# Optimization experiments

Measured on AMD Instinct MI355X. Metric: run time of the kernel, lower is better.

The kernel has to match this reference:

```python
import jax, jax.numpy as jnp
import numpy as np

B, C, F_, T = 128, 8, 58, 249
RES_C = 24  # out_c * len('fct')


def conv1d(x, w, b, stride):
    # x: (B, Cin, L), w: (Cout, Cin, K)
    y = jax.lax.conv_general_dilated(x, w, (stride,), 'VALID',
                                     dimension_numbers=('NCH', 'OIH', 'NCH'))
    return y + b[None, :, None]


def attend(Q, K, V):
    # torch: softmax(Q @ K^T / sqrt(d_q), dim=1) @ V   (softmax over ROWS, dim=1)
    d = Q.shape[-1]
    scores = jnp.einsum('bnd,bmd->bnm', Q, K) / jnp.sqrt(jnp.asarray(d, Q.dtype))
    alpha = jax.nn.softmax(scores, axis=1)
    return jnp.einsum('bnm,bml->bnl', alpha, V)


def dyrelub(x, w1, b1, w2, b2):
    # standard DyReLU-B, k=2: coefs from global-avg-pooled features
    b_, c_ = x.shape[0], x.shape[1]
    theta = x.mean(axis=(2, 3))                       # (B, C)
    h = jax.nn.relu(theta @ w1.T + b1)
    theta = 2.0 * jax.nn.sigmoid(h @ w2.T + b2) - 1.0  # (B, 4C)
    lambdas = jnp.array([1.0, 1.0, 0.5, 0.5], dtype=x.dtype)
    init_v = jnp.array([1.0, 0.0, 0.0, 0.0], dtype=x.dtype)
    coefs = theta.reshape(b_, c_, 4) * lambdas + init_v  # (B,C,4)
    a = coefs[:, :, None, None, :2]
    bb = coefs[:, :, None, None, 2:]
    return jnp.max(x[..., None] * a + bb, axis=-1)


def setup_inputs():
    key = jax.random.key(0)
    ks = iter(jax.random.split(key, 48))

    def rn(shape, s=0.1):
        return jax.random.normal(next(ks), shape, dtype=jnp.float32) * s

    return {
        'x': jax.random.normal(next(ks), (B, C, F_, T), dtype=jnp.float32),
        'inp': jax.random.normal(next(ks), (B, 1, F_ + 2, T + 2), dtype=jnp.float32),
        'w_diff': rn((C, C)), 'b_diff': rn((C,)),
        'w_res': rn((RES_C, 1, 3, 3)), 'b_res': rn((RES_C,)),
        'bn_gamma': jnp.ones((RES_C,), jnp.float32), 'bn_beta': jnp.zeros((RES_C,), jnp.float32),
        'bn_mean': rn((RES_C,)),
        'bn_var': jax.random.uniform(next(ks), (RES_C,), jnp.float32, 0.5, 1.5),
        'dy_w1': rn((6, RES_C)), 'dy_b1': rn((6,)),
        'dy_w2': rn((4 * RES_C, 6)), 'dy_b2': rn((4 * RES_C,)),
        'wq': rn((C, C)), 'bq': rn((C,)),
        'wk': rn((C, C)), 'bk': rn((C,)),
        'fq0_w': rn((F_, F_, 1)), 'fq0_b': rn((F_,)),
        'fk0_w': rn((F_, F_, 1)), 'fk0_b': rn((F_,)),
        'cq0_w': rn((C, C, 1)), 'cq0_b': rn((C,)),
        'ck0_w': rn((C, C, 1)), 'ck0_b': rn((C,)),
        'tq0_w': rn((T, T, 1)), 'tq0_b': rn((T,)),
        'tk0_w': rn((T, T, 1)), 'tk0_b': rn((T,)),
        'tq1_w': rn((T, T, 2)), 'tq1_b': rn((T,)),
        'tk1_w': rn((T, T, 2)), 'tk1_b': rn((T,)),
    }


def reference(x, inp, w_diff, b_diff, w_res, b_res, bn_gamma, bn_beta, bn_mean, bn_var,
              dy_w1, dy_b1, dy_w2, dy_b2, wq, bq, wk, bk,
              fq0_w, fq0_b, fk0_w, fk0_b, cq0_w, cq0_b, ck0_w, ck0_b,
              tq0_w, tq0_b, tk0_w, tk0_b, tq1_w, tq1_b, tk1_w, tk1_b):
    Bx = x.shape[0]
    # ---- differ branch (temporal difference via 1x1 conv) ----
    x_t_fea = x[..., :-1]                 # (B,C,F,T-1)
    first_t = x[..., :1]                  # (B,C,F,1)
    x_conv = jnp.einsum('oc,bcft->boft', w_diff, x) + b_diff[None, :, None, None]
    x_query = x_conv[..., 1:] - x_t_fea
    differ = jnp.concatenate([first_t, x_query], axis=-1)  # (B,C,F,T)

    # ---- residual branch: conv3x3 -> BN(eval) -> DyReLU-B ----
    xr = jax.lax.conv_general_dilated(inp, w_res, (1, 1), 'VALID',
                                      dimension_numbers=('NCHW', 'OIHW', 'NCHW'))
    xr = xr + b_res[None, :, None, None]
    inv = jax.lax.rsqrt(bn_var + 1e-5)
    xr = (xr - bn_mean[None, :, None, None]) * (inv * bn_gamma)[None, :, None, None] \
         + bn_beta[None, :, None, None]
    xr = dyrelub(xr, dy_w1, dy_b1, dy_w2, dy_b2)   # (B,24,F,T)

    # ---- multi-view multi-scale attention ----
    Q = jnp.einsum('oc,bcft->boft', wq, differ) + bq[None, :, None, None]
    K = jnp.einsum('oc,bcft->boft', wk, differ) + bk[None, :, None, None]
    V = differ

    # f view: raw reshape (B,C,F,T) -> (B,F,C*T)
    Qf = Q.reshape(Bx, F_, C * T); Kf = K.reshape(Bx, F_, C * T); Vf = V.reshape(Bx, F_, C * T)
    a_f = attend(Qf, Kf, Vf)
    a_f = a_f + attend(conv1d(Qf, fq0_w, fq0_b, 1), conv1d(Kf, fk0_w, fk0_b, 1), Vf)
    a_f = a_f.reshape(Bx, C, F_, T)

    # c view: (B,C,F*T)
    Qc = Q.reshape(Bx, C, F_ * T); Kc = K.reshape(Bx, C, F_ * T); Vc = V.reshape(Bx, C, F_ * T)
    a_c = attend(Qc, Kc, Vc)
    a_c = a_c + attend(conv1d(Qc, cq0_w, cq0_b, 1), conv1d(Kc, ck0_w, ck0_b, 1), Vc)
    a_c = a_c.reshape(Bx, C, F_, T)

    # t view: (B,T,C*F)
    Qt = Q.reshape(Bx, T, C * F_); Kt = K.reshape(Bx, T, C * F_); Vt = V.reshape(Bx, T, C * F_)
    a_t = attend(Qt, Kt, Vt)
    a_t = a_t + attend(conv1d(Qt, tq0_w, tq0_b, 1), conv1d(Kt, tk0_w, tk0_b, 1), Vt)
    a_t = a_t + attend(conv1d(Qt, tq1_w, tq1_b, 2), conv1d(Kt, tk1_w, tk1_b, 2), Vt)
    a_t = a_t.reshape(Bx, C, F_, T)

    atten_differ = jnp.concatenate([a_f, a_c, a_t], axis=1)  # (B,24,F,T)
    return atten_differ + xr
```

## Files before the change

kernel.cpp:

```cpp
#include <hip/hip_runtime.h>
#include <cmath>

#define Bn   128
#define Cn   8
#define Fn   58
#define Tn   249
#define RCn  24
#define FT   14442
#define CFT  115536
#define OUTB 346608
#define IH   60
#define IW   251

__global__ void k_differ_qk(const float* __restrict__ x,
                            const float* __restrict__ w_diff, const float* __restrict__ b_diff,
                            const float* __restrict__ wq, const float* __restrict__ bq,
                            const float* __restrict__ wk, const float* __restrict__ bk,
                            float* __restrict__ V, float* __restrict__ Q, float* __restrict__ K) {
    int gid = blockIdx.x * blockDim.x + threadIdx.x;
    if (gid >= Bn * FT) return;
    int b  = gid / FT;
    int ft = gid % FT;
    int t  = ft % Tn;
    const float* xb = x + (size_t)b * CFT + ft;

    float xv[Cn], d[Cn];
    #pragma unroll
    for (int c = 0; c < Cn; c++) xv[c] = xb[c * FT];

    if (t == 0) {
        #pragma unroll
        for (int c = 0; c < Cn; c++) d[c] = xv[c];
    } else {
        #pragma unroll
        for (int o = 0; o < Cn; o++) {
            float s = b_diff[o];
            #pragma unroll
            for (int c = 0; c < Cn; c++) s += w_diff[o * Cn + c] * xv[c];
            d[o] = s - xb[o * FT - 1];
        }
    }

    float* Vb = V + (size_t)b * CFT + ft;
    float* Qb = Q + (size_t)b * CFT + ft;
    float* Kb = K + (size_t)b * CFT + ft;
    #pragma unroll
    for (int o = 0; o < Cn; o++) {
        Vb[o * FT] = d[o];
        float q = bq[o], k = bk[o];
        #pragma unroll
        for (int c = 0; c < Cn; c++) { q += wq[o * Cn + c] * d[c]; k += wk[o * Cn + c] * d[c]; }
        Qb[o * FT] = q;
        Kb[o * FT] = k;
    }
}

template<int AN, int RG, int GW, int VL>
__global__ void __launch_bounds__(256, 4)
k_gemm(const float* __restrict__ A, long long aStride, int aLd,
       const float* __restrict__ bias,
       const float* __restrict__ V, long long vStride, int dv,
       float* __restrict__ out, long long oStride, int add,
       int gx, int gy)
{
    constexpr int TPG = 256 / GW;
    constexpr int RGA = (RG + 3) & ~3;
    constexpr int RGP = GW * RGA + 4;
    __shared__ float As[64][RGP];

    int nblk = gridDim.x;
    int bid  = blockIdx.x;
    if ((nblk & 7) == 0) {
        int cpx = nblk >> 3;
        bid = (bid & 7) * cpx + (bid >> 3);
    }
    int gxy = gx * gy;
    int b   = bid / gxy;
    int rem = bid - b * gxy;
    int jb  = (rem / gx) * (GW * RG);
    int g   = threadIdx.x / TPG;
    int cl  = threadIdx.x % TPG;
    int j0  = jb + g * RG;
    int l   = (rem % gx) * (TPG * VL) + cl * VL;
    bool act = (l + VL <= dv);

    const float* Ab = A + (size_t)b * aStride;
    const float* Vb = V + (size_t)b * vStride + l;

    float acc[RG][VL];
    #pragma unroll
    for (int j = 0; j < RG; j++)
        #pragma unroll
        for (int e = 0; e < VL; e++) acc[j][e] = 0.f;

    for (int m0 = 0; m0 < AN; m0 += 64) {
        int mc = min(64, AN - m0);
        for (int idx = threadIdx.x; idx < GW * RG * 64; idx += 256) {
            int j = idx >> 6, mi = idx & 63;
            float w = 0.f;
            if (jb + j < AN && mi < mc) w = Ab[(size_t)(jb + j) * aLd + m0 + mi];
            As[mi][(j / RG) * RGA + (j % RG)] = w;
        }
        __syncthreads();
        if (act) {
            const float* Vp = Vb + (size_t)m0 * dv;
            auto LD = [&](int i) -> float4 {
                const float* p = Vp + (size_t)min(i, mc - 1) * dv;
                if constexpr (VL == 4) {
                    return *(const float4*)p;
                } else {
                    float2 t = *(const float2*)p;
                    return make_float4(t.x, t.y, 0.f, 0.f);
                }
            };
            auto FMA = [&](int mm, float4 x) {
                const float* w = &As[mm][g * RGA];
                #pragma unroll
                for (int j = 0; j < RG; j++) {
                    float wv = w[j];
                    acc[j][0] += wv * x.x;
                    if constexpr (VL >= 2) acc[j][1] += wv * x.y;
                    if constexpr (VL >= 4) {
                        acc[j][2] += wv * x.z;
                        acc[j][3] += wv * x.w;
                    }
                }
            };
            float4 p0 = LD(0), p1 = LD(1), p2 = LD(2), p3 = LD(3);
            int mm = 0;
            for (; mm + 4 <= mc; mm += 4) {
                FMA(mm + 0, p0); p0 = LD(mm + 4);
                FMA(mm + 1, p1); p1 = LD(mm + 5);
                FMA(mm + 2, p2); p2 = LD(mm + 6);
                FMA(mm + 3, p3); p3 = LD(mm + 7);
            }
            if (mm     < mc) FMA(mm,     p0);
            if (mm + 1 < mc) FMA(mm + 1, p1);
            if (mm + 2 < mc) FMA(mm + 2, p2);
        }
        __syncthreads();
    }

    if (!act) return;
    float* ob = out + (size_t)b * oStride + l;
    #pragma unroll
    for (int j = 0; j < RG; j++) {
        if (j0 + j < AN) {
            float bv = bias ? bias[j0 + j] : 0.f;
            float* op = ob + (size_t)(j0 + j) * dv;
            if (add) {
                #pragma unroll
                for (int e = 0; e < VL; e++) op[e] += acc[j][e] + bv;
            } else {
                if constexpr (VL == 4) {
                    *(float4*)op = make_float4(acc[j][0] + bv, acc[j][1] + bv,
                                               acc[j][2] + bv, acc[j][3] + bv);
                } else {
                    *(float2*)op = make_float2(acc[j][0] + bv, acc[j][1] + bv);
                }
            }
        }
    }
}

template<int AN, int RGW>
__global__ void __launch_bounds__(256, 4)
k_gemm_s2d(const float* __restrict__ Wa, const float* __restrict__ ba,
           const float* __restrict__ Xa, float* __restrict__ Oa,
           const float* __restrict__ Wb, const float* __restrict__ bb_,
           const float* __restrict__ Xb_, float* __restrict__ Ob,
           long long xStride, int d_in, int d_out, long long oStride, int gy)
{
    constexpr int BR = 4 * RGW;
    __shared__ float Ws[64][2 * BR + 4];

    int nblk = gridDim.x;
    int bid  = blockIdx.x;
    if ((nblk & 7) == 0) {
        int cpx = nblk >> 3;
        bid = (bid & 7) * cpx + (bid >> 3);
    }
    int half = (bid >= Bn * gy);
    if (half) bid -= Bn * gy;
    const float* W    = half ? Wb  : Wa;
    const float* bias = half ? bb_ : ba;
    const float* X    = half ? Xb_ : Xa;
    float*       Og   = half ? Ob  : Oa;

    int b    = bid / gy;
    int jb   = (bid % gy) * BR;
    int w    = threadIdx.x >> 6;
    int lane = threadIdx.x & 63;
    int j0   = jb + w * RGW;
    int l4   = lane * 4;
    bool act = l4 < d_out;

    const float* Xb = X + (size_t)b * xStride + 2 * l4;

    float acc[RGW][4];
    #pragma unroll
    for (int j = 0; j < RGW; j++)
        #pragma unroll
        for (int e = 0; e < 4; e++) acc[j][e] = 0.f;

    for (int m0 = 0; m0 < AN; m0 += 64) {
        int mc = min(64, AN - m0);
        for (int idx = threadIdx.x; idx < 2 * BR * 64; idx += 256) {
            int mi = idx & 63, rest = idx >> 6;
            int rj = rest >> 1, tap = rest & 1;
            float wv = 0.f;
            if (jb + rj < AN && mi < mc)
                wv = W[((size_t)(jb + rj) * AN + m0 + mi) * 2 + tap];
            Ws[mi][2 * rj + tap] = wv;
        }
        __syncthreads();
        if (act) {
            const float* Xp = Xb + (size_t)m0 * d_in;
            auto FMAS = [&](int mm, float4 x0, float4 x1) {
                const float* wrow = &Ws[mm][2 * (w * RGW)];
                #pragma unroll
                for (int j = 0; j < RGW; j++) {
                    float w0 = wrow[2 * j], w1 = wrow[2 * j + 1];
                    acc[j][0] += w0 * x0.x + w1 * x0.y;
                    acc[j][1] += w0 * x0.z + w1 * x0.w;
                    acc[j][2] += w0 * x1.x + w1 * x1.y;
                    acc[j][3] += w0 * x1.z + w1 * x1.w;
                }
            };
            if (mc == 64) {
                auto LDU = [&](int i, float4& a, float4& bb) {
                    const float* p = Xp + (size_t)i * d_in;
                    a = *(const float4*)p; bb = *(const float4*)(p + 4);
                };
                float4 a0, b0, a1, b1, a2, b2, a3, b3;
                LDU(0, a0, b0); LDU(1, a1, b1); LDU(2, a2, b2); LDU(3, a3, b3);
                int mm = 0;
                for (; mm < 60; mm += 4) {
                    FMAS(mm + 0, a0, b0); LDU(mm + 4, a0, b0);
                    FMAS(mm + 1, a1, b1); LDU(mm + 5, a1, b1);
                    FMAS(mm + 2, a2, b2); LDU(mm + 6, a2, b2);
                    FMAS(mm + 3, a3, b3); LDU(mm + 7, a3, b3);
                }
                FMAS(60, a0, b0); FMAS(61, a1, b1);
                FMAS(62, a2, b2); FMAS(63, a3, b3);
            } else {
                auto LDP = [&](int i, float4& a, float4& bb) {
                    const float* p = Xp + (size_t)min(i, mc - 1) * d_in;
                    a = *(const float4*)p; bb = *(const float4*)(p + 4);
                };
                float4 a0, b0, a1, b1, a2, b2, a3, b3;
                LDP(0, a0, b0); LDP(1, a1, b1); LDP(2, a2, b2); LDP(3, a3, b3);
                int mm = 0;
                for (; mm + 4 <= mc; mm += 4) {
                    FMAS(mm + 0, a0, b0); LDP(mm + 4, a0, b0);
                    FMAS(mm + 1, a1, b1); LDP(mm + 5, a1, b1);
                    FMAS(mm + 2, a2, b2); LDP(mm + 6, a2, b2);
                    FMAS(mm + 3, a3, b3); LDP(mm + 7, a3, b3);
                }
                if (mm     < mc) FMAS(mm,     a0, b0);
                if (mm + 1 < mc) FMAS(mm + 1, a1, b1);
                if (mm + 2 < mc) FMAS(mm + 2, a2, b2);
            }
        }
        __syncthreads();
    }

    if (!act) return;
    float* ob = Og + (size_t)b * oStride + l4;
    #pragma unroll
    for (int j = 0; j < RGW; j++) {
        if (j0 + j < AN) {
            float bv = bias[j0 + j];
            *(float4*)(ob + (size_t)(j0 + j) * d_out) =
                make_float4(acc[j][0] + bv, acc[j][1] + bv,
                            acc[j][2] + bv, acc[j][3] + bv);
        }
    }
}

__global__ void __launch_bounds__(256, 4)
k_scores128(const float* __restrict__ Q, const float* __restrict__ K,
            float* __restrict__ S, int n, int d, int sQ) {
    __shared__ float Qs[16][132];
    __shared__ float Ks[16][132];
    int b  = blockIdx.z;
    int r0 = blockIdx.x * 128, c0 = blockIdx.y * 128;
    int tid = threadIdx.x;
    int tx = tid & 15, ty = tid >> 4;
    int lrow = tid >> 1;
    int lk   = (tid & 1) * 8;
    const float* Qr = Q + (size_t)b * sQ + (size_t)min(r0 + lrow, n - 1) * d;
    const float* Kr = K + (size_t)b * sQ + (size_t)min(c0 + lrow, n - 1) * d;

    float acc[8][8] = {};
    for (int kk = 0; kk < d; kk += 16) {
        #pragma unroll
        for (int h = 0; h < 2; h++) {
            int g = kk + lk + h * 4;
            float4 qv = make_float4(0.f, 0.f, 0.f, 0.f);
            float4 kv = make_float4(0.f, 0.f, 0.f, 0.f);
            if (g + 4 <= d) {
                qv = *(const float4*)(Qr + g);
                kv = *(const float4*)(Kr + g);
            }
            int kb = lk + h * 4;
            Qs[kb + 0][lrow] = qv.x; Qs[kb + 1][lrow] = qv.y;
            Qs[kb + 2][lrow] = qv.z; Qs[kb + 3][lrow] = qv.w;
            Ks[kb + 0][lrow] = kv.x; Ks[kb + 1][lrow] = kv.y;
            Ks[kb + 2][lrow] = kv.z; Ks[kb + 3][lrow] = kv.w;
        }
        __syncthreads();
        #pragma unroll
        for (int k = 0; k < 16; k++) {
            float4 qa = *(const float4*)&Qs[k][ty * 8];
            float4 qb = *(const float4*)&Qs[k][ty * 8 + 4];
            float4 ka = *(const float4*)&Ks[k][tx * 8];
            float4 kb4 = *(const float4*)&Ks[k][tx * 8 + 4];
            float aq[8] = {qa.x, qa.y, qa.z, qa.w, qb.x, qb.y, qb.z, qb.w};
            float ak[8] = {ka.x, ka.y, ka.z, ka.w, kb4.x, kb4.y, kb4.z, kb4.w};
            #pragma unroll
            for (int i = 0; i < 8; i++)
                #pragma unroll
                for (int j = 0; j < 8; j++) acc[i][j] += aq[i] * ak[j];
        }
        __syncthreads();
    }
    float* Sb = S + (size_t)b * n * n;
    #pragma unroll
    for (int i = 0; i < 8; i++) {
        int r = r0 + ty * 8 + i;
        if (r < n) {
            #pragma unroll
            for (int j = 0; j < 8; j++) {
                int c = c0 + tx * 8 + j;
                if (c < n) Sb[(size_t)r * n + c] = acc[i][j];
            }
        }
    }
}

__global__ void __launch_bounds__(256)
k_scores_sk(const float* __restrict__ Q, const float* __restrict__ K,
            float* __restrict__ SP, int n, int d, int kz_n, int chunk, int sQ) {
    __shared__ float Qs[16][68];
    __shared__ float Ks[16][68];
    int bz = blockIdx.z;
    int b  = bz / kz_n, kz = bz % kz_n;
    int k0 = kz * chunk, k1 = min(d, k0 + chunk);
    int r0 = blockIdx.x * 64, c0 = blockIdx.y * 64;
    int tx = threadIdx.x & 15, ty = threadIdx.x >> 4;
    int lrow = threadIdx.x >> 2;
    int lk   = (threadIdx.x & 3) * 4;
    const float* Qr = Q + (size_t)b * sQ + (size_t)min(r0 + lrow, n - 1) * d;
    const float* Kr = K + (size_t)b * sQ + (size_t)min(c0 + lrow, n - 1) * d;
    bool qok = (r0 + lrow) < n;
    bool kok = (c0 + lrow) < n;
    float acc[4][4] = {};

    for (int kk = k0; kk < k1; kk += 16) {
        #pragma unroll
        for (int u = 0; u < 4; u++) {
            int gk = kk + lk + u;
            bool gv = gk < k1;
            Qs[lk + u][lrow] = (qok && gv) ? Qr[gk] : 0.f;
            Ks[lk + u][lrow] = (kok && gv) ? Kr[gk] : 0.f;
        }
        __syncthreads();
        #pragma unroll
        for (int k = 0; k < 16; k++) {
            float4 q4 = *(const float4*)&Qs[k][ty * 4];
            float4 k4 = *(const float4*)&Ks[k][tx * 4];
            float aq[4] = {q4.x, q4.y, q4.z, q4.w};
            float ak[4] = {k4.x, k4.y, k4.z, k4.w};
            #pragma unroll
            for (int i = 0; i < 4; i++)
                #pragma unroll
                for (int j = 0; j < 4; j++) acc[i][j] += aq[i] * ak[j];
        }
        __syncthreads();
    }
    float* Sb = SP + (size_t)bz * n * n;
    #pragma unroll
    for (int i = 0; i < 4; i++) {
        int r = r0 + ty * 4 + i;
        #pragma unroll
        for (int j = 0; j < 4; j++) {
            int c = c0 + tx * 4 + j;
            if (r < n && c < n) Sb[(size_t)r * n + c] = acc[i][j];
        }
    }
}

__global__ void __launch_bounds__(256)
k_abt(const float* __restrict__ A, long long aBatch, int aLd,
      const float* __restrict__ B, int bLd,
      float* __restrict__ O, long long oBatch, int oLd,
      int n, int d)
{
    __shared__ float Qs[16][68];
    __shared__ float Ks[16][68];
    int b  = blockIdx.z;
    int r0 = blockIdx.x * 64, c0 = blockIdx.y * 64;
    int tx = threadIdx.x & 15, ty = threadIdx.x >> 4;
    int lrow = threadIdx.x >> 2;
    int lk   = (threadIdx.x & 3) * 4;
    const float* Ar = A + (size_t)b * aBatch + (size_t)min(r0 + lrow, n - 1) * aLd;
    const float* Br = B + (size_t)min(c0 + lrow, n - 1) * bLd;
    bool aok = (r0 + lrow) < n;
    bool bok = (c0 + lrow) < n;
    float acc[4][4] = {};

    for (int kk = 0; kk < d; kk += 16) {
        #pragma unroll
        for (int u = 0; u < 4; u++) {
            int gk = kk + lk + u;
            bool gv = gk < d;
            Qs[lk + u][lrow] = (aok && gv) ? Ar[gk] : 0.f;
            Ks[lk + u][lrow] = (bok && gv) ? Br[gk] : 0.f;
        }
        __syncthreads();
        #pragma unroll
        for (int k = 0; k < 16; k++) {
            float4 q4 = *(const float4*)&Qs[k][ty * 4];
            float4 k4 = *(const float4*)&Ks[k][tx * 4];
            float aq[4] = {q4.x, q4.y, q4.z, q4.w};
            float ak[4] = {k4.x, k4.y, k4.z, k4.w};
            #pragma unroll
            for (int i = 0; i < 4; i++)
                #pragma unroll
                for (int j = 0; j < 4; j++) acc[i][j] += aq[i] * ak[j];
        }
        __syncthreads();
    }
    #pragma unroll
    for (int i = 0; i < 4; i++) {
        int r = r0 + ty * 4 + i;
        #pragma unroll
        for (int j = 0; j < 4; j++) {
            int c = c0 + tx * 4 + j;
            if (r < n && c < oLd)
                O[(size_t)b * oBatch + (size_t)r * oLd + c] = (c < n) ? acc[i][j] : 0.f;
        }
    }
}

__global__ void k_rowsum2(const float* __restrict__ Q, const float* __restrict__ K,
                          int n, int d, float* __restrict__ sQ, float* __restrict__ sK) {
    int b = blockIdx.x / n, r = blockIdx.x % n;
    const float* q = Q + (size_t)b * CFT + (size_t)r * d;
    const float* k = K + (size_t)b * CFT + (size_t)r * d;
    float s1 = 0.f, s2 = 0.f;
    for (int i = threadIdx.x; i < d; i += 256) { s1 += q[i]; s2 += k[i]; }
    __shared__ float red[2][256];
    red[0][threadIdx.x] = s1; red[1][threadIdx.x] = s2;
    __syncthreads();
    for (int s = 128; s > 0; s >>= 1) {
        if (threadIdx.x < s) {
            red[0][threadIdx.x] += red[0][threadIdx.x + s];
            red[1][threadIdx.x] += red[1][threadIdx.x + s];
        }
        __syncthreads();
    }
    if (threadIdx.x == 0) {
        sQ[(size_t)b * n + r] = red[0][0];
        sK[(size_t)b * n + r] = red[1][0];
    }
}

__global__ void __launch_bounds__(256)
k_matvec2(const float* __restrict__ Wq, const float* __restrict__ Wk,
          const float* __restrict__ sQ, const float* __restrict__ sK,
          float* __restrict__ u, float* __restrict__ v, int n) {
    int b = blockIdx.x;
    __shared__ float sq[256], sk[256];
    for (int i = threadIdx.x; i < n; i += 256) {
        sq[i] = sQ[(size_t)b * n + i];
        sk[i] = sK[(size_t)b * n + i];
    }
    __syncthreads();
    for (int r = threadIdx.x; r < n; r += 256) {
        float a = 0.f, bb = 0.f;
        for (int m = 0; m < n; m++) {
            a  += Wq[(size_t)r * n + m] * sq[m];
            bb += Wk[(size_t)r * n + m] * sk[m];
        }
        u[(size_t)b * n + r] = a;
        v[(size_t)b * n + r] = bb;
    }
}

__global__ void k_scombine(const float* __restrict__ SP, float* __restrict__ S,
                           int n, int kz_n) {
    int idx = blockIdx.x * 256 + threadIdx.x;
    int nn = n * n;
    if (idx >= Bn * nn) return;
    int b = idx / nn, rc = idx % nn;
    float s = 0.f;
    for (int kz = 0; kz < kz_n; kz++) s += SP[((size_t)b * kz_n + kz) * nn + rc];
    S[(size_t)b * nn + rc] = s;
}

#define C_LZ 8
__global__ void k_gram8(const float* __restrict__ Q, const float* __restrict__ K,
                        float* __restrict__ SP) {
    int b  = blockIdx.x / C_LZ;
    int lz = blockIdx.x % C_LZ;
    int g  = threadIdx.x >> 6;
    int p  = threadIdx.x & 63;
    int r  = p >> 3, c = p & 7;
    const float* Qb = Q + (size_t)b * CFT + (size_t)r * FT;
    const float* Kb = K + (size_t)b * CFT + (size_t)c * FT;
    int chunk = (FT + C_LZ - 1) / C_LZ;
    int l0 = lz * chunk, l1 = min(FT, l0 + chunk);
    float acc = 0.f;
    for (int l = l0 + g; l < l1; l += 4) acc += Qb[l] * Kb[l];
    __shared__ float red[256];
    red[threadIdx.x] = acc;
    __syncthreads();
    if (threadIdx.x < 64) {
        float s = red[p] + red[64 + p] + red[128 + p] + red[192 + p];
        SP[(size_t)blockIdx.x * 64 + p] = s;
    }
}

__global__ void __launch_bounds__(256)
k_softmax(float* __restrict__ S, long long sBatch, int ldS,
          float* __restrict__ Sacc, long long aBatch,
          int n, int cb, float scale, int first,
          const float* __restrict__ bq, const float* __restrict__ u,
          const float* __restrict__ vv, const float* __restrict__ bk,
          float dlen) {
    __shared__ float red[4][64];
    int b  = blockIdx.x / cb;
    int tc = threadIdx.x & 63;
    int g  = threadIdx.x >> 6;
    int c  = (blockIdx.x % cb) * 64 + tc;
    bool act = c < n;
    float* Sb = S + (size_t)b * sBatch;
    bool r1 = (bq != nullptr);
    const float* ub = r1 ? u + (size_t)b * n : nullptr;
    float alpha = 0.f, beta = 0.f;
    if (r1 && act) {
        beta  = bk[c];
        alpha = vv[(size_t)b * n + c] + dlen * beta;
    }
    auto VAL = [&](int r) {
        float s = Sb[(size_t)r * ldS + c];
        if (r1) s += bq[r] * alpha + ub[r] * beta;
        return s;
    };

    float mx = -1e30f;
    if (act) for (int r = g; r < n; r += 4) mx = fmaxf(mx, VAL(r));
    red[g][tc] = mx;
    __syncthreads();
    mx = fmaxf(fmaxf(red[0][tc], red[1][tc]), fmaxf(red[2][tc], red[3][tc]));
    __syncthreads();

    float sum = 0.f;
    if (act) {
        if (Sacc) {
            for (int r = g; r < n; r += 4) sum += __expf((VAL(r) - mx) * scale);
        } else {
            for (int r = g; r < n; r += 4) {
                float e = __expf((VAL(r) - mx) * scale);
                Sb[(size_t)r * ldS + c] = e;
                sum += e;
            }
        }
    }
    red[g][tc] = sum;
    __syncthreads();
    float inv = 1.f / (red[0][tc] + red[1][tc] + red[2][tc] + red[3][tc]);
    if (act) {
        if (Sacc) {
            float* Ab = Sacc + (size_t)b * aBatch;
            for (int r = g; r < n; r += 4) {
                float e = __expf((VAL(r) - mx) * scale) * inv;
                size_t o = (size_t)r * n + c;
                Ab[o] = first ? e : (Ab[o] + e);
            }
        } else {
            for (int r = g; r < n; r += 4) Sb[(size_t)r * ldS + c] *= inv;
        }
    }
}

__global__ void k_mean(const float* __restrict__ inp, const float* __restrict__ w_res,
                       const float* __restrict__ b_res, const float* __restrict__ bn_gamma,
                       const float* __restrict__ bn_beta, const float* __restrict__ bn_mean,
                       const float* __restrict__ bn_var, float* __restrict__ meanbuf) {
    int b  = blockIdx.x / RCn;
    int rc = blockIdx.x % RCn;
    float w[9];
    #pragma unroll
    for (int i = 0; i < 9; i++) w[i] = w_res[rc * 9 + i];
    float g    = bn_gamma[rc] * rsqrtf(bn_var[rc] + 1e-5f);
    float bias = (b_res[rc] - bn_mean[rc]) * g + bn_beta[rc];
    const float* ib = inp + (size_t)b * IH * IW;

    float sum = 0.f;
    for (int idx = threadIdx.x; idx < FT; idx += 256) {
        int f = idx / Tn, t = idx % Tn;
        const float* p = ib + f * IW + t;
        float v = w[0]*p[0]     + w[1]*p[1]     + w[2]*p[2]
                + w[3]*p[IW]    + w[4]*p[IW+1]  + w[5]*p[IW+2]
                + w[6]*p[2*IW]  + w[7]*p[2*IW+1]+ w[8]*p[2*IW+2];
        sum += v * g + bias;
    }
    __shared__ float red[256];
    red[threadIdx.x] = sum;
    __syncthreads();
    for (int s = 128; s > 0; s >>= 1) {
        if (threadIdx.x < s) red[threadIdx.x] += red[threadIdx.x + s];
        __syncthreads();
    }
    if (threadIdx.x == 0) meanbuf[b * RCn + rc] = red[0] / (float)FT;
}

__global__ void k_coef(const float* __restrict__ meanbuf, const float* __restrict__ w1,
                       const float* __restrict__ b1, const float* __restrict__ w2,
                       const float* __restrict__ b2, float* __restrict__ coef) {
    int b = blockIdx.x;
    int k = threadIdx.x;
    if (k >= 4 * RCn) return;
    const float* th = meanbuf + b * RCn;
    float h[6];
    #pragma unroll
    for (int j = 0; j < 6; j++) {
        float s = b1[j];
        #pragma unroll
        for (int c = 0; c < RCn; c++) s += th[c] * w1[j * RCn + c];
        h[j] = fmaxf(s, 0.f);
    }
    float s = b2[k];
    #pragma unroll
    for (int j = 0; j < 6; j++) s += h[j] * w2[k * 6 + j];
    float g2 = 2.f / (1.f + __expf(-s)) - 1.f;
    const float lam[4] = {1.f, 1.f, 0.5f, 0.5f};
    const float ini[4] = {1.f, 0.f, 0.f, 0.f};
    coef[b * 96 + k] = g2 * lam[k & 3] + ini[k & 3];
}

__global__ void k_xr_add(const float* __restrict__ inp, const float* __restrict__ w_res,
                         const float* __restrict__ b_res, const float* __restrict__ bn_gamma,
                         const float* __restrict__ bn_beta, const float* __restrict__ bn_mean,
                         const float* __restrict__ bn_var, const float* __restrict__ coef,
                         float* __restrict__ out) {
    int gid = blockIdx.x * blockDim.x + threadIdx.x;
    if (gid >= Bn * RCn * FT) return;
    int t   = gid % Tn;
    int tmp = gid / Tn;
    int f   = tmp % Fn;  tmp /= Fn;
    int rc  = tmp % RCn;
    int b   = tmp / RCn;

    const float* wp = w_res + rc * 9;
    float g    = bn_gamma[rc] * rsqrtf(bn_var[rc] + 1e-5f);
    float bias = (b_res[rc] - bn_mean[rc]) * g + bn_beta[rc];
    const float* p = inp + (size_t)b * IH * IW + f * IW + t;
    float v = wp[0]*p[0]    + wp[1]*p[1]      + wp[2]*p[2]
            + wp[3]*p[IW]   + wp[4]*p[IW+1]   + wp[5]*p[IW+2]
            + wp[6]*p[2*IW] + wp[7]*p[2*IW+1] + wp[8]*p[2*IW+2];
    float xv = v * g + bias;

    const float* cf = coef + ((size_t)b * RCn + rc) * 4;
    float r = fmaxf(xv * cf[0] + cf[2], xv * cf[1] + cf[3]);
    out[gid] += r;
}

extern "C" void kernel_launch(void* const* d_in, const int* in_sizes, int n_in,
                              void* d_out, int out_size, void* d_ws, size_t ws_size,
                              hipStream_t stream) {
    const float* x        = (const float*)d_in[0];
    const float* inp      = (const float*)d_in[1];
    const float* w_diff   = (const float*)d_in[2];
    const float* b_diff   = (const float*)d_in[3];
    const float* w_res    = (const float*)d_in[4];
    const float* b_res    = (const float*)d_in[5];
    const float* bn_gamma = (const float*)d_in[6];
    const float* bn_beta  = (const float*)d_in[7];
    const float* bn_mean  = (const float*)d_in[8];
    const float* bn_var   = (const float*)d_in[9];
    const float* dy_w1    = (const float*)d_in[10];
    const float* dy_b1    = (const float*)d_in[11];
    const float* dy_w2    = (const float*)d_in[12];
    const float* dy_b2    = (const float*)d_in[13];
    const float* wq       = (const float*)d_in[14];
    const float* bq       = (const float*)d_in[15];
    const float* wk       = (const float*)d_in[16];
    const float* bk       = (const float*)d_in[17];
    const float* fq0_w    = (const float*)d_in[18];
    const float* fq0_b    = (const float*)d_in[19];
    const float* fk0_w    = (const float*)d_in[20];
    const float* fk0_b    = (const float*)d_in[21];
    const float* cq0_w    = (const float*)d_in[22];
    const float* cq0_b    = (const float*)d_in[23];
    const float* ck0_w    = (const float*)d_in[24];
    const float* ck0_b    = (const float*)d_in[25];
    const float* tq0_w    = (const float*)d_in[26];
    const float* tq0_b    = (const float*)d_in[27];
    const float* tk0_w    = (const float*)d_in[28];
    const float* tk0_b    = (const float*)d_in[29];
    const float* tq1_w    = (const float*)d_in[30];
    const float* tq1_b    = (const float*)d_in[31];
    const float* tk1_w    = (const float*)d_in[32];
    const float* tk1_b    = (const float*)d_in[33];

    float* out = (float*)d_out;
    float* ws  = (float*)d_ws;

    const size_t NB  = (size_t)Bn * CFT;
    const size_t SNN = (size_t)Bn * Tn * Tn;
    float* V       = ws;
    float* Q       = ws + NB;
    float* K       = ws + 2 * NB;
    float* Qp      = ws + 3 * NB;
    float* Kp      = ws + 4 * NB;
    float* S       = ws + 5 * NB;
    float* meanbuf = S + SNN;
    float* coef    = meanbuf + 3072;
    float* SaccT   = coef + 12288;
    float* T2f   = S + 1000000;
    float* S2f   = S + 2000000;
    float* SaccF = S + 3000000;
    float* SaccC = S + 3500000;
    float* SPp   = S + 4000000;
    float* sg    = Kp + 9000000;
    float *sQt = sg,          *sKt = sg + 32000,  *ut = sg + 64000,  *vt = sg + 96000;
    float *sQf = sg + 128000, *sKf = sg + 136000, *uf = sg + 144000, *vf = sg + 152000;
    float *sQc = sg + 160000, *sKc = sg + 161024, *uc = sg + 162048, *vc = sg + 163072;
    bool fuseT = ws_size >= (5 * NB + 2 * SNN + 15360) * sizeof(float);

    {
        int total = Bn * FT;
        k_differ_qk<<<dim3((total + 255) / 256), dim3(256), 0, stream>>>(
            x, w_diff, b_diff, wq, bq, wk, bk, V, Q, K);
    }

    const float scF   = 1.0f / sqrtf(1992.f);
    const float scC   = 1.0f / sqrtf((float)FT);
    const float sc464 = 1.0f / sqrtf(464.f);
    const float sc232 = 1.0f / sqrtf(232.f);

    {
        dim3 g1(1, 1, Bn * 8);
        k_scores_sk<<<g1, dim3(256), 0, stream>>>(Q, K, SPp, Fn, 1992, 8, 256, CFT);
        k_scombine<<<dim3((Bn * Fn * Fn + 255) / 256), dim3(256), 0, stream>>>(SPp, S, Fn, 8);
        k_rowsum2<<<dim3(Bn * Fn), dim3(256), 0, stream>>>(Q, K, Fn, 1992, sQf, sKf);
        k_matvec2<<<dim3(Bn), dim3(256), 0, stream>>>(fq0_w, fk0_w, sQf, sKf, uf, vf, Fn);
        k_abt<<<dim3(1, 1, Bn), dim3(256), 0, stream>>>(S, 3364, Fn, fk0_w, Fn,
                                                        T2f, 3480, 60, Fn, Fn);
        k_gemm<Fn, 8, 4, 4><<<dim3(Bn * 2), dim3(256), 0, stream>>>(
            fq0_w, 0, Fn, nullptr, T2f, 3480, 60, S2f, 3480, 0, 1, 2);
        k_softmax<<<dim3(Bn), dim3(256), 0, stream>>>(
            S, 3364, Fn, SaccF, 3364, Fn, 1, scF, 1, nullptr, nullptr, nullptr, nullptr, 0.f);
        k_softmax<<<dim3(Bn), dim3(256), 0, stream>>>(
            S2f, 3480, 60, SaccF, 3364, Fn, 1, scF, 0, fq0_b, uf, vf, fk0_b, 1992.f);
        k_gemm<Fn, 15, 2, 4><<<dim3(Bn * 8), dim3(256), 0, stream>>>(
            SaccF, 3364, Fn, nullptr, V, CFT, 1992, out, OUTB, 0, 4, 2);
    }

    {
        k_gram8<<<dim3(Bn * C_LZ), dim3(256), 0, stream>>>(Q, K, SPp);
        k_scombine<<<dim3((Bn * 64 + 255) / 256), dim3(256), 0, stream>>>(SPp, S, Cn, C_LZ);
        k_rowsum2<<<dim3(Bn * Cn), dim3(256), 0, stream>>>(Q, K, Cn, FT, sQc, sKc);
        k_matvec2<<<dim3(Bn), dim3(256), 0, stream>>>(cq0_w, ck0_w, sQc, sKc, uc, vc, Cn);
        k_abt<<<dim3(1, 1, Bn), dim3(256), 0, stream>>>(S, 64, Cn, ck0_w, Cn,
                                                        T2f, 64, 8, Cn, Cn);
        k_gemm<Cn, 8, 1, 2><<<dim3(Bn), dim3(256), 0, stream>>>(
            cq0_w, 0, Cn, nullptr, T2f, 64, 8, S2f, 64, 0, 1, 1);
        k_softmax<<<dim3(Bn), dim3(256), 0, stream>>>(
            S, 64, Cn, SaccC, 64, Cn, 1, scC, 1, nullptr, nullptr, nullptr, nullptr, 0.f);
        k_softmax<<<dim3(Bn), dim3(256), 0, stream>>>(
            S2f, 64, 8, SaccC, 64, Cn, 1, scC, 0, cq0_b, uc, vc, ck0_b, (float)FT);
        k_gemm<Cn, 8, 1, 2><<<dim3(Bn * 29), dim3(256), 0, stream>>>(
            SaccC, 64, Cn, nullptr, V, CFT, FT, out + CFT, OUTB, 0, 29, 1);
    }

    {
        k_scores128<<<dim3(2, 2, Bn), dim3(256), 0, stream>>>(Q, K, S, Tn, 464, CFT);
        k_rowsum2<<<dim3(Bn * Tn), dim3(256), 0, stream>>>(Q, K, Tn, 464, sQt, sKt);
        k_matvec2<<<dim3(Bn), dim3(256), 0, stream>>>(tq0_w, tk0_w, sQt, sKt, ut, vt, Tn);
        k_abt<<<dim3(4, 4, Bn), dim3(256), 0, stream>>>(S, 62001, Tn, tk0_w, Tn,
                                                        Qp, 62748, 252, Tn, Tn);
        k_gemm<Tn, 8, 4, 4><<<dim3(Bn * 8), dim3(256), 0, stream>>>(
            tq0_w, 0, Tn, nullptr, Qp, 62748, 252, Kp, 62748, 0, 1, 8);
        if (fuseT) {
            k_softmax<<<dim3(Bn * 4), dim3(256), 0, stream>>>(
                S, 62001, Tn, SaccT, 62001, Tn, 4, sc464, 1,
                nullptr, nullptr, nullptr, nullptr, 0.f);
            k_softmax<<<dim3(Bn * 4), dim3(256), 0, stream>>>(
                Kp, 62748, 252, SaccT, 62001, Tn, 4, sc464, 0,
                tq0_b, ut, vt, tk0_b, 464.f);
            k_gemm_s2d<Tn, 4><<<dim3(2 * Bn * 16), dim3(256), 0, stream>>>(
                tq1_w, tq1_b, Q, Qp, tk1_w, tk1_b, K, Kp,
                CFT, 464, 232, (long long)Tn * 232, 16);
            k_scores128<<<dim3(2, 2, Bn), dim3(256), 0, stream>>>(Qp, Kp, S, Tn, 232, Tn * 232);
            k_softmax<<<dim3(Bn * 4), dim3(256), 0, stream>>>(
                S, 62001, Tn, SaccT, 62001, Tn, 4, sc232, 0,
                nullptr, nullptr, nullptr, nullptr, 0.f);
            k_gemm<Tn, 16, 2, 4><<<dim3(Bn * 8), dim3(256), 0, stream>>>(
                SaccT, 62001, Tn, nullptr, V, CFT, 464, out + 2 * CFT, OUTB, 0, 1, 8);
        } else {
            k_softmax<<<dim3(Bn * 4), dim3(256), 0, stream>>>(
                S, 62001, Tn, nullptr, 0, Tn, 4, sc464, 0,
                nullptr, nullptr, nullptr, nullptr, 0.f);
            k_gemm<Tn, 16, 2, 4><<<dim3(Bn * 8), dim3(256), 0, stream>>>(
                S, 62001, Tn, nullptr, V, CFT, 464, out + 2 * CFT, OUTB, 0, 1, 8);
            k_softmax<<<dim3(Bn * 4), dim3(256), 0, stream>>>(
                Kp, 62748, 252, nullptr, 0, Tn, 4, sc464, 0,
                tq0_b, ut, vt, tk0_b, 464.f);
            k_gemm<Tn, 16, 2, 4><<<dim3(Bn * 8), dim3(256), 0, stream>>>(
                Kp, 62748, 252, nullptr, V, CFT, 464, out + 2 * CFT, OUTB, 1, 1, 8);
            k_gemm_s2d<Tn, 4><<<dim3(2 * Bn * 16), dim3(256), 0, stream>>>(
                tq1_w, tq1_b, Q, Qp, tk1_w, tk1_b, K, Kp,
                CFT, 464, 232, (long long)Tn * 232, 16);
            k_scores128<<<dim3(2, 2, Bn), dim3(256), 0, stream>>>(Qp, Kp, S, Tn, 232, Tn * 232);
            k_softmax<<<dim3(Bn * 4), dim3(256), 0, stream>>>(
                S, 62001, Tn, nullptr, 0, Tn, 4, sc232, 0,
                nullptr, nullptr, nullptr, nullptr, 0.f);
            k_gemm<Tn, 16, 2, 4><<<dim3(Bn * 8), dim3(256), 0, stream>>>(
                S, 62001, Tn, nullptr, V, CFT, 464, out + 2 * CFT, OUTB, 1, 1, 8);
        }
    }

    k_mean<<<dim3(Bn * RCn), dim3(256), 0, stream>>>(
        inp, w_res, b_res, bn_gamma, bn_beta, bn_mean, bn_var, meanbuf);
    k_coef<<<dim3(Bn), dim3(128), 0, stream>>>(meanbuf, dy_w1, dy_b1, dy_w2, dy_b2, coef);
    {
        int total = Bn * RCn * FT;
        k_xr_add<<<dim3((total + 255) / 256), dim3(256), 0, stream>>>(
            inp, w_res, b_res, bn_gamma, bn_beta, bn_mean, bn_var, coef, out);
    }
}
```

Before: 2.232 ms.

## Fuse paired softmaxes, add 128-tile ABt kernel, split s2d GEMM, drop load clamps

Merges the two column-softmax passes that accumulate into the same buffer into one kernel that reads both score matrices and writes the summed probabilities once. Replaces the ABt kernel for the t-view projection with a 128x128-tiled version using 8x8 register blocks. Splits the combined Q/K stride-2 GEMM into two separate launches, and removes the min() clamps on tail-row loads in the GEMM kernels. The unclamped loads may read beyond valid rows or past buffer ends.

```diff
diff --git a/kernel.cpp b/kernel.cpp
--- a/kernel.cpp
+++ b/kernel.cpp
@@ -105,7 +105,7 @@
         if (act) {
             const float* Vp = Vb + (size_t)m0 * dv;
             auto LD = [&](int i) -> float4 {
-                const float* p = Vp + (size_t)min(i, mc - 1) * dv;
+                const float* p = Vp + (size_t)i * dv;
                 if constexpr (VL == 4) {
                     return *(const float4*)p;
                 } else {
@@ -165,11 +165,9 @@
 
 template<int AN, int RGW>
 __global__ void __launch_bounds__(256, 4)
-k_gemm_s2d(const float* __restrict__ Wa, const float* __restrict__ ba,
-           const float* __restrict__ Xa, float* __restrict__ Oa,
-           const float* __restrict__ Wb, const float* __restrict__ bb_,
-           const float* __restrict__ Xb_, float* __restrict__ Ob,
-           long long xStride, int d_in, int d_out, long long oStride, int gy)
+k_gemm_s2(const float* __restrict__ W, const float* __restrict__ bias,
+          const float* __restrict__ X, long long xStride, int d_in, int d_out,
+          float* __restrict__ out, long long oStride, int gy)
 {
     constexpr int BR = 4 * RGW;
     __shared__ float Ws[64][2 * BR + 4];
@@ -180,13 +178,6 @@
         int cpx = nblk >> 3;
         bid = (bid & 7) * cpx + (bid >> 3);
     }
-    int half = (bid >= Bn * gy);
-    if (half) bid -= Bn * gy;
-    const float* W    = half ? Wb  : Wa;
-    const float* bias = half ? bb_ : ba;
-    const float* X    = half ? Xb_ : Xa;
-    float*       Og   = half ? Ob  : Oa;
-
     int b    = bid / gy;
     int jb   = (bid % gy) * BR;
     int w    = threadIdx.x >> 6;
@@ -227,29 +218,23 @@
                     acc[j][3] += w0 * x1.z + w1 * x1.w;
                 }
             };
+            auto LDP = [&](int i, float4& a, float4& bb) {
+                const float* p = Xp + (size_t)i * d_in;
+                a = *(const float4*)p; bb = *(const float4*)(p + 4);
+            };
+            float4 a0, b0, a1, b1, a2, b2, a3, b3;
+            LDP(0, a0, b0); LDP(1, a1, b1); LDP(2, a2, b2); LDP(3, a3, b3);
             if (mc == 64) {
-                auto LDU = [&](int i, float4& a, float4& bb) {
-                    const float* p = Xp + (size_t)i * d_in;
-                    a = *(const float4*)p; bb = *(const float4*)(p + 4);
-                };
-                float4 a0, b0, a1, b1, a2, b2, a3, b3;
-                LDU(0, a0, b0); LDU(1, a1, b1); LDU(2, a2, b2); LDU(3, a3, b3);
                 int mm = 0;
                 for (; mm < 60; mm += 4) {
-                    FMAS(mm + 0, a0, b0); LDU(mm + 4, a0, b0);
-                    FMAS(mm + 1, a1, b1); LDU(mm + 5, a1, b1);
-                    FMAS(mm + 2, a2, b2); LDU(mm + 6, a2, b2);
-                    FMAS(mm + 3, a3, b3); LDU(mm + 7, a3, b3);
+                    FMAS(mm + 0, a0, b0); LDP(mm + 4, a0, b0);
+                    FMAS(mm + 1, a1, b1); LDP(mm + 5, a1, b1);
+                    FMAS(mm + 2, a2, b2); LDP(mm + 6, a2, b2);
+                    FMAS(mm + 3, a3, b3); LDP(mm + 7, a3, b3);
                 }
                 FMAS(60, a0, b0); FMAS(61, a1, b1);
                 FMAS(62, a2, b2); FMAS(63, a3, b3);
             } else {
-                auto LDP = [&](int i, float4& a, float4& bb) {
-                    const float* p = Xp + (size_t)min(i, mc - 1) * d_in;
-                    a = *(const float4*)p; bb = *(const float4*)(p + 4);
-                };
-                float4 a0, b0, a1, b1, a2, b2, a3, b3;
-                LDP(0, a0, b0); LDP(1, a1, b1); LDP(2, a2, b2); LDP(3, a3, b3);
                 int mm = 0;
                 for (; mm + 4 <= mc; mm += 4) {
                     FMAS(mm + 0, a0, b0); LDP(mm + 4, a0, b0);
@@ -266,7 +251,7 @@
     }
 
     if (!act) return;
-    float* ob = Og + (size_t)b * oStride + l4;
+    float* ob = out + (size_t)b * oStride + l4;
     #pragma unroll
     for (int j = 0; j < RGW; j++) {
         if (j0 + j < AN) {
@@ -334,6 +319,77 @@
             for (int j = 0; j < 8; j++) {
                 int c = c0 + tx * 8 + j;
                 if (c < n) Sb[(size_t)r * n + c] = acc[i][j];
+            }
+        }
+    }
+}
+
+__global__ void __launch_bounds__(256, 4)
+k_abt128(const float* __restrict__ A, long long aBatch, int aLd,
+         const float* __restrict__ B, int bLd,
+         float* __restrict__ O, long long oBatch, int oLd, int n, int d) {
+    __shared__ float Qs[16][132];
+    __shared__ float Ks[16][132];
+    int b  = blockIdx.z;
+    int r0 = blockIdx.x * 128, c0 = blockIdx.y * 128;
+    int tid = threadIdx.x;
+    int tx = tid & 15, ty = tid >> 4;
+    int lrow = tid >> 1;
+    int lk   = (tid & 1) * 8;
+    const float* Ar = A + (size_t)b * aBatch + (size_t)min(r0 + lrow, n - 1) * aLd;
+    const float* Br = B + (size_t)min(c0 + lrow, n - 1) * bLd;
+
+    float acc[8][8] = {};
+    for (int kk = 0; kk < d; kk += 16) {
+        #pragma unroll
+        for (int h = 0; h < 2; h++) {
+            int g = kk + lk + h * 4;
+            float4 av, bv;
+            if (g + 4 <= d) {
+                av = *(const float4*)(Ar + g);
+                bv = *(const float4*)(Br + g);
+            } else {
+                float ae[4], be[4];
+                #pragma unroll
+                for (int e = 0; e < 4; e++) {
+                    int gg = g + e;
+                    ae[e] = (gg < d) ? Ar[gg] : 0.f;
+                    be[e] = (gg < d) ? Br[gg] : 0.f;
+                }
+                av = make_float4(ae[0], ae[1], ae[2], ae[3]);
+                bv = make_float4(be[0], be[1], be[2], be[3]);
+            }
+            int kb = lk + h * 4;
+            Qs[kb + 0][lrow] = av.x; Qs[kb + 1][lrow] = av.y;
+            Qs[kb + 2][lrow] = av.z; Qs[kb + 3][lrow] = av.w;
+            Ks[kb + 0][lrow] = bv.x; Ks[kb + 1][lrow] = bv.y;
+            Ks[kb + 2][lrow] = bv.z; Ks[kb + 3][lrow] = bv.w;
+        }
+        __syncthreads();
+        #pragma unroll
+        for (int k = 0; k < 16; k++) {
+            float4 qa = *(const float4*)&Qs[k][ty * 8];
+            float4 qb = *(const float4*)&Qs[k][ty * 8 + 4];
+            float4 ka = *(const float4*)&Ks[k][tx * 8];
+            float4 kb4 = *(const float4*)&Ks[k][tx * 8 + 4];
+            float aq[8] = {qa.x, qa.y, qa.z, qa.w, qb.x, qb.y, qb.z, qb.w};
+            float ak[8] = {ka.x, ka.y, ka.z, ka.w, kb4.x, kb4.y, kb4.z, kb4.w};
+            #pragma unroll
+            for (int i = 0; i < 8; i++)
+                #pragma unroll
+                for (int j = 0; j < 8; j++) acc[i][j] += aq[i] * ak[j];
+        }
+        __syncthreads();
+    }
+    #pragma unroll
+    for (int i = 0; i < 8; i++) {
+        int r = r0 + ty * 8 + i;
+        if (r < n) {
+            #pragma unroll
+            for (int j = 0; j < 8; j++) {
+                int c = c0 + tx * 8 + j;
+                if (c < oLd)
+                    O[(size_t)b * oBatch + (size_t)r * oLd + c] = (c < n) ? acc[i][j] : 0.f;
             }
         }
     }
@@ -520,6 +576,59 @@
     if (threadIdx.x < 64) {
         float s = red[p] + red[64 + p] + red[128 + p] + red[192 + p];
         SP[(size_t)blockIdx.x * 64 + p] = s;
+    }
+}
+
+__global__ void __launch_bounds__(256)
+k_softmax2(const float* __restrict__ S1, long long b1, int ld1,
+           const float* __restrict__ S2, long long b2, int ld2,
+           float* __restrict__ Sacc, long long aB,
+           int n, int cb, float scale,
+           const float* __restrict__ bq, const float* __restrict__ u,
+           const float* __restrict__ vv, const float* __restrict__ bk, float dlen) {
+    __shared__ float redA[4][64];
+    __shared__ float redB[4][64];
+    int b  = blockIdx.x / cb;
+    int tc = threadIdx.x & 63;
+    int g  = threadIdx.x >> 6;
+    int c  = (blockIdx.x % cb) * 64 + tc;
+    bool act = c < n;
+    const float* A1 = S1 + (size_t)b * b1;
+    const float* A2 = S2 + (size_t)b * b2;
+    const float* ub = u + (size_t)b * n;
+    float alpha = 0.f, beta = 0.f;
+    if (act) {
+        beta  = bk[c];
+        alpha = vv[(size_t)b * n + c] + dlen * beta;
+    }
+    auto V1 = [&](int r) { return A1[(size_t)r * ld1 + c]; };
+    auto V2 = [&](int r) { return A2[(size_t)r * ld2 + c] + bq[r] * alpha + ub[r] * beta; };
+
+    float m1 = -1e30f, m2 = -1e30f;
+    if (act) for (int r = g; r < n; r += 4) {
+        m1 = fmaxf(m1, V1(r)); m2 = fmaxf(m2, V2(r));
+    }
+    redA[g][tc] = m1; redB[g][tc] = m2;
+    __syncthreads();
+    m1 = fmaxf(fmaxf(redA[0][tc], redA[1][tc]), fmaxf(redA[2][tc], redA[3][tc]));
+    m2 = fmaxf(fmaxf(redB[0][tc], redB[1][tc]), fmaxf(redB[2][tc], redB[3][tc]));
+    __syncthreads();
+
+    float s1 = 0.f, s2 = 0.f;
+    if (act) for (int r = g; r < n; r += 4) {
+        s1 += __expf((V1(r) - m1) * scale);
+        s2 += __expf((V2(r) - m2) * scale);
+    }
+    redA[g][tc] = s1; redB[g][tc] = s2;
+    __syncthreads();
+    float i1 = 1.f / (redA[0][tc] + redA[1][tc] + redA[2][tc] + redA[3][tc]);
+    float i2 = 1.f / (redB[0][tc] + redB[1][tc] + redB[2][tc] + redB[3][tc]);
+    if (act) {
+        float* Ab = Sacc + (size_t)b * aB;
+        for (int r = g; r < n; r += 4) {
+            Ab[(size_t)r * n + c] = __expf((V1(r) - m1) * scale) * i1
+                                  + __expf((V2(r) - m2) * scale) * i2;
+        }
     }
 }
 
@@ -753,10 +862,9 @@
                                                         T2f, 3480, 60, Fn, Fn);
         k_gemm<Fn, 8, 4, 4><<<dim3(Bn * 2), dim3(256), 0, stream>>>(
             fq0_w, 0, Fn, nullptr, T2f, 3480, 60, S2f, 3480, 0, 1, 2);
-        k_softmax<<<dim3(Bn), dim3(256), 0, stream>>>(
-            S, 3364, Fn, SaccF, 3364, Fn, 1, scF, 1, nullptr, nullptr, nullptr, nullptr, 0.f);
-        k_softmax<<<dim3(Bn), dim3(256), 0, stream>>>(
-            S2f, 3480, 60, SaccF, 3364, Fn, 1, scF, 0, fq0_b, uf, vf, fk0_b, 1992.f);
+        k_softmax2<<<dim3(Bn), dim3(256), 0, stream>>>(
+            S, 3364, Fn, S2f, 3480, 60, SaccF, 3364, Fn, 1, scF,
+            fq0_b, uf, vf, fk0_b, 1992.f);
         k_gemm<Fn, 15, 2, 4><<<dim3(Bn * 8), dim3(256), 0, stream>>>(
             SaccF, 3364, Fn, nullptr, V, CFT, 1992, out, OUTB, 0, 4, 2);
     }
@@ -770,10 +878,9 @@
                                                         T2f, 64, 8, Cn, Cn);
         k_gemm<Cn, 8, 1, 2><<<dim3(Bn), dim3(256), 0, stream>>>(
             cq0_w, 0, Cn, nullptr, T2f, 64, 8, S2f, 64, 0, 1, 1);
-        k_softmax<<<dim3(Bn), dim3(256), 0, stream>>>(
-            S, 64, Cn, SaccC, 64, Cn, 1, scC, 1, nullptr, nullptr, nullptr, nullptr, 0.f);
-        k_softmax<<<dim3(Bn), dim3(256), 0, stream>>>(
-            S2f, 64, 8, SaccC, 64, Cn, 1, scC, 0, cq0_b, uc, vc, ck0_b, (float)FT);
+        k_softmax2<<<dim3(Bn), dim3(256), 0, stream>>>(
+            S, 64, Cn, S2f, 64, 8, SaccC, 64, Cn, 1, scC,
+            cq0_b, uc, vc, ck0_b, (float)FT);
         k_gemm<Cn, 8, 1, 2><<<dim3(Bn * 29), dim3(256), 0, stream>>>(
             SaccC, 64, Cn, nullptr, V, CFT, FT, out + CFT, OUTB, 0, 29, 1);
     }
@@ -782,20 +889,18 @@
         k_scores128<<<dim3(2, 2, Bn), dim3(256), 0, stream>>>(Q, K, S, Tn, 464, CFT);
         k_rowsum2<<<dim3(Bn * Tn), dim3(256), 0, stream>>>(Q, K, Tn, 464, sQt, sKt);
         k_matvec2<<<dim3(Bn), dim3(256), 0, stream>>>(tq0_w, tk0_w, sQt, sKt, ut, vt, Tn);
-        k_abt<<<dim3(4, 4, Bn), dim3(256), 0, stream>>>(S, 62001, Tn, tk0_w, Tn,
-                                                        Qp, 62748, 252, Tn, Tn);
+        k_abt128<<<dim3(2, 2, Bn), dim3(256), 0, stream>>>(S, 62001, Tn, tk0_w, Tn,
+                                                           Qp, 62748, 252, Tn, Tn);
         k_gemm<Tn, 8, 4, 4><<<dim3(Bn * 8), dim3(256), 0, stream>>>(
             tq0_w, 0, Tn, nullptr, Qp, 62748, 252, Kp, 62748, 0, 1, 8);
         if (fuseT) {
-            k_softmax<<<dim3(Bn * 4), dim3(256), 0, stream>>>(
-                S, 62001, Tn, SaccT, 62001, Tn, 4, sc464, 1,
-                nullptr, nullptr, nullptr, nullptr, 0.f);
-            k_softmax<<<dim3(Bn * 4), dim3(256), 0, stream>>>(
-                Kp, 62748, 252, SaccT, 62001, Tn, 4, sc464, 0,
+            k_softmax2<<<dim3(Bn * 4), dim3(256), 0, stream>>>(
+                S, 62001, Tn, Kp, 62748, 252, SaccT, 62001, Tn, 4, sc464,
                 tq0_b, ut, vt, tk0_b, 464.f);
-            k_gemm_s2d<Tn, 4><<<dim3(2 * Bn * 16), dim3(256), 0, stream>>>(
-                tq1_w, tq1_b, Q, Qp, tk1_w, tk1_b, K, Kp,
-                CFT, 464, 232, (long long)Tn * 232, 16);
+            k_gemm_s2<Tn, 4><<<dim3(Bn * 16), dim3(256), 0, stream>>>(
+                tq1_w, tq1_b, Q, CFT, 464, 232, Qp, (long long)Tn * 232, 16);
+            k_gemm_s2<Tn, 4><<<dim3(Bn * 16), dim3(256), 0, stream>>>(
+                tk1_w, tk1_b, K, CFT, 464, 232, Kp, (long long)Tn * 232, 16);
             k_scores128<<<dim3(2, 2, Bn), dim3(256), 0, stream>>>(Qp, Kp, S, Tn, 232, Tn * 232);
             k_softmax<<<dim3(Bn * 4), dim3(256), 0, stream>>>(
                 S, 62001, Tn, SaccT, 62001, Tn, 4, sc232, 0,
@@ -813,9 +918,10 @@
                 tq0_b, ut, vt, tk0_b, 464.f);
             k_gemm<Tn, 16, 2, 4><<<dim3(Bn * 8), dim3(256), 0, stream>>>(
                 Kp, 62748, 252, nullptr, V, CFT, 464, out + 2 * CFT, OUTB, 1, 1, 8);
-            k_gemm_s2d<Tn, 4><<<dim3(2 * Bn * 16), dim3(256), 0, stream>>>(
-                tq1_w, tq1_b, Q, Qp, tk1_w, tk1_b, K, Kp,
-                CFT, 464, 232, (long long)Tn * 232, 16);
+            k_gemm_s2<Tn, 4><<<dim3(Bn * 16), dim3(256), 0, stream>>>(
+                tq1_w, tq1_b, Q, CFT, 464, 232, Qp, (long long)Tn * 232, 16);
+            k_gemm_s2<Tn, 4><<<dim3(Bn * 16), dim3(256), 0, stream>>>(
+                tk1_w, tk1_b, K, CFT, 464, 232, Kp, (long long)Tn * 232, 16);
             k_scores128<<<dim3(2, 2, Bn), dim3(256), 0, stream>>>(Qp, Kp, S, Tn, 232, Tn * 232);
             k_softmax<<<dim3(Bn * 4), dim3(256), 0, stream>>>(
                 S, 62001, Tn, nullptr, 0, Tn, 4, sc232, 0,
```

Measured after the change: 2.389 ms. 1.07x slower.
